# Performance work log

Measured on AMD Instinct MI355X. Metric: run time of the kernel, lower is better.

Reference implementation:

```python
import jax, jax.numpy as jnp
import numpy as np

B, N, C = 4, 4096, 2048
EPS = 1e-5  # torch.nn.LayerNorm default


def setup_inputs() -> dict:
    key = jax.random.key(0)
    kx, = jax.random.split(key, 1)
    x = jax.random.normal(kx, (B, N, C), dtype=jnp.float32)
    gamma = jnp.ones((C,), dtype=jnp.float32)   # LayerNorm weight
    beta = jnp.zeros((C,), dtype=jnp.float32)   # LayerNorm bias
    return {"x": x, "gamma": gamma, "beta": beta}


def reference(x, gamma, beta):
    # The original repeats x to (B,N,N,C), applies a (no-op on the diagonal)
    # triu mask, FFTs every row over C, and extracts the (n,n) diagonal.
    # The diagonal rows are exactly the unmasked originals, so this equals:
    #   LayerNorm(real(fft(x, axis=-1)))
    y = jnp.fft.fft(x, axis=-1).real  # (B,N,C)
    mu = jnp.mean(y, axis=-1, keepdims=True)
    var = jnp.mean(jnp.square(y - mu), axis=-1, keepdims=True)  # biased, as torch LN
    return (y - mu) * jax.lax.rsqrt(var + EPS) * gamma + beta
```

## Files before the change

kernel.cpp:

```cpp
#include <hip/hip_runtime.h>
#include <math.h>


#define TPB 256
#define CD  2048

template<int N_, int S_>
__device__ __forceinline__ void r4_stage(const float2* __restrict__ src,
                                         float2* __restrict__ dst, int t)
{
    const float theta0 = -6.28318530717958647692f / (float)N_;
#pragma unroll
    for (int it = 0; it < 2; ++it) {
        const int b = t + TPB * it;
        const int q = b & (S_ - 1);
        const int p = b / S_;
        float2 x0 = src[b];
        float2 x1 = src[b + 512];
        float2 x2 = src[b + 1024];
        float2 x3 = src[b + 1536];
        float apc_r = x0.x + x2.x, apc_i = x0.y + x2.y;
        float amc_r = x0.x - x2.x, amc_i = x0.y - x2.y;
        float bpd_r = x1.x + x3.x, bpd_i = x1.y + x3.y;
        float bmd_r = x1.x - x3.x, bmd_i = x1.y - x3.y;
        float t0r = apc_r + bpd_r, t0i = apc_i + bpd_i;
        float t2r = apc_r - bpd_r, t2i = apc_i - bpd_i;
        float t1r = amc_r + bmd_i, t1i = amc_i - bmd_r;
        float t3r = amc_r - bmd_i, t3i = amc_i + bmd_r;
        float s1, c1;
        __sincosf(theta0 * (float)p, &s1, &c1);
        const float c2 = c1 * c1 - s1 * s1, s2 = 2.0f * c1 * s1;
        const float c3 = c1 * c2 - s1 * s2, s3 = c1 * s2 + s1 * c2;
        const int o = q + 4 * S_ * p;
        dst[o]          = make_float2(t0r, t0i);
        dst[o + S_]     = make_float2(c1 * t1r - s1 * t1i, c1 * t1i + s1 * t1r);
        dst[o + 2 * S_] = make_float2(c2 * t2r - s2 * t2i, c2 * t2i + s2 * t2r);
        dst[o + 3 * S_] = make_float2(c3 * t3r - s3 * t3i, c3 * t3i + s3 * t3r);
    }
}

__global__ __launch_bounds__(TPB) void fourier_ln_kernel(
    const float* __restrict__ x,
    const float* __restrict__ gamma,
    const float* __restrict__ beta,
    float* __restrict__ out)
{
    __shared__ float2 bufA[CD];
    __shared__ float2 bufB[CD];

    const int t = threadIdx.x;
    const long long row0 = 2LL * (long long)blockIdx.x;
    const long long row1 = row0 + 1;

    const float4* x0 = (const float4*)(x + row0 * CD);
    const float4* x1 = (const float4*)(x + row1 * CD);
#pragma unroll
    for (int i = 0; i < 2; i++) {
        int idx = t + TPB * i;
        float4 a = x0[idx];
        float4 b = x1[idx];
        int base = 4 * idx;
        bufA[base + 0] = make_float2(a.x, b.x);
        bufA[base + 1] = make_float2(a.y, b.y);
        bufA[base + 2] = make_float2(a.z, b.z);
        bufA[base + 3] = make_float2(a.w, b.w);
    }
    __syncthreads();

    r4_stage<2048, 1>(bufA, bufB, t);  __syncthreads();
    r4_stage< 512, 4>(bufB, bufA, t);  __syncthreads();
    r4_stage< 128, 16>(bufA, bufB, t); __syncthreads();
    r4_stage<  32, 64>(bufB, bufA, t); __syncthreads();
    r4_stage<   8, 256>(bufA, bufB, t); __syncthreads();

#pragma unroll
    for (int it = 0; it < 4; ++it) {
        int b = t + TPB * it;
        float2 u = bufB[b];
        float2 v = bufB[b + 1024];
        bufA[b]        = make_float2(u.x + v.x, u.y + v.y);
        bufA[b + 1024] = make_float2(u.x - v.x, u.y - v.y);
    }
    __syncthreads();

    float y0v[8], y1v[8];
    float s0 = 0.f, ss0 = 0.f, s1 = 0.f, ss1 = 0.f;
#pragma unroll
    for (int i = 0; i < 8; i++) {
        int k = t + TPB * i;
        int rv = (CD - k) & (CD - 1);
        float2 zk = bufA[k];
        float2 zr = bufA[rv];
        float a = 0.5f * (zk.x + zr.x);
        float b = 0.5f * (zk.y + zr.y);
        y0v[i] = a; y1v[i] = b;
        s0 += a; ss0 += a * a;
        s1 += b; ss1 += b * b;
    }

#pragma unroll
    for (int off = 32; off > 0; off >>= 1) {
        s0  += __shfl_down(s0,  off, 64);
        ss0 += __shfl_down(ss0, off, 64);
        s1  += __shfl_down(s1,  off, 64);
        ss1 += __shfl_down(ss1, off, 64);
    }
    float* rmem = (float*)bufB;
    const int wave = t >> 6;
    if ((t & 63) == 0) {
        rmem[4 * wave + 0] = s0;
        rmem[4 * wave + 1] = ss0;
        rmem[4 * wave + 2] = s1;
        rmem[4 * wave + 3] = ss1;
    }
    __syncthreads();
    if (t == 0) {
        float S0 = 0.f, SS0 = 0.f, S1 = 0.f, SS1 = 0.f;
#pragma unroll
        for (int w = 0; w < 4; w++) {
            S0  += rmem[4 * w + 0];
            SS0 += rmem[4 * w + 1];
            S1  += rmem[4 * w + 2];
            SS1 += rmem[4 * w + 3];
        }
        const float inv = 1.0f / (float)CD;
        float mu0 = S0 * inv, mu1 = S1 * inv;
        float v0 = SS0 * inv - mu0 * mu0;
        float v1 = SS1 * inv - mu1 * mu1;
        rmem[16] = mu0; rmem[17] = rsqrtf(v0 + 1e-5f);
        rmem[18] = mu1; rmem[19] = rsqrtf(v1 + 1e-5f);
    }
    __syncthreads();
    const float mu0 = rmem[16], r0 = rmem[17];
    const float mu1 = rmem[18], r1 = rmem[19];

    float* o0 = out + row0 * CD;
    float* o1 = out + row1 * CD;
#pragma unroll
    for (int i = 0; i < 8; i++) {
        int k = t + TPB * i;
        float g = gamma[k], be = beta[k];
        o0[k] = (y0v[i] - mu0) * r0 * g + be;
        o1[k] = (y1v[i] - mu1) * r1 * g + be;
    }
}

extern "C" void kernel_launch(void* const* d_in, const int* in_sizes, int n_in,
                              void* d_out, int out_size, void* d_ws, size_t ws_size,
                              hipStream_t stream) {
    (void)in_sizes; (void)n_in; (void)d_ws; (void)ws_size; (void)out_size;
    const float* x     = (const float*)d_in[0];
    const float* gamma = (const float*)d_in[1];
    const float* beta  = (const float*)d_in[2];
    float* out = (float*)d_out;

    const int total_rows = 4 * 4096;
    const int blocks = total_rows / 2;
    fourier_ln_kernel<<<blocks, TPB, 0, stream>>>(x, gamma, beta, out);
}
```

Measured before the change: 231.5 us.

## Replace radix-4 shared-memory FFT with register radix-8 stages and padded LDS

Swaps the five radix-4 stages plus a radix-2 pass, each bouncing through two shared buffers, for three radix-8 register butterflies and a final radix-8 pass (4+2 split). Data moves through one padded shared buffer so LDS accesses avoid bank conflicts. Output and gamma/beta accesses are vectorized to float4, and launch bounds request higher occupancy. The aim is fewer LDS passes and barriers and less shared memory per block, at the cost of more registers per thread and more intricate index math.

```diff
diff --git a/kernel.cpp b/kernel.cpp
--- a/kernel.cpp
+++ b/kernel.cpp
@@ -5,97 +5,135 @@
 #define TPB 256
 #define CD  2048
 
-template<int N_, int S_>
-__device__ __forceinline__ void r4_stage(const float2* __restrict__ src,
-                                         float2* __restrict__ dst, int t)
+__device__ __forceinline__ float2 cadd(float2 a, float2 b){ return make_float2(a.x+b.x, a.y+b.y); }
+__device__ __forceinline__ float2 csub(float2 a, float2 b){ return make_float2(a.x-b.x, a.y-b.y); }
+
+__device__ __forceinline__ void dft8(const float2* z, float2* y)
 {
-    const float theta0 = -6.28318530717958647692f / (float)N_;
-#pragma unroll
-    for (int it = 0; it < 2; ++it) {
-        const int b = t + TPB * it;
-        const int q = b & (S_ - 1);
-        const int p = b / S_;
-        float2 x0 = src[b];
-        float2 x1 = src[b + 512];
-        float2 x2 = src[b + 1024];
-        float2 x3 = src[b + 1536];
-        float apc_r = x0.x + x2.x, apc_i = x0.y + x2.y;
-        float amc_r = x0.x - x2.x, amc_i = x0.y - x2.y;
-        float bpd_r = x1.x + x3.x, bpd_i = x1.y + x3.y;
-        float bmd_r = x1.x - x3.x, bmd_i = x1.y - x3.y;
-        float t0r = apc_r + bpd_r, t0i = apc_i + bpd_i;
-        float t2r = apc_r - bpd_r, t2i = apc_i - bpd_i;
-        float t1r = amc_r + bmd_i, t1i = amc_i - bmd_r;
-        float t3r = amc_r - bmd_i, t3i = amc_i + bmd_r;
-        float s1, c1;
-        __sincosf(theta0 * (float)p, &s1, &c1);
-        const float c2 = c1 * c1 - s1 * s1, s2 = 2.0f * c1 * s1;
-        const float c3 = c1 * c2 - s1 * s2, s3 = c1 * s2 + s1 * c2;
-        const int o = q + 4 * S_ * p;
-        dst[o]          = make_float2(t0r, t0i);
-        dst[o + S_]     = make_float2(c1 * t1r - s1 * t1i, c1 * t1i + s1 * t1r);
-        dst[o + 2 * S_] = make_float2(c2 * t2r - s2 * t2i, c2 * t2i + s2 * t2r);
-        dst[o + 3 * S_] = make_float2(c3 * t3r - s3 * t3i, c3 * t3i + s3 * t3r);
+    const float C8 = 0.70710678118654752440f;
+    float2 a0=cadd(z[0],z[4]), a1=cadd(z[1],z[5]), a2=cadd(z[2],z[6]), a3=cadd(z[3],z[7]);
+    float2 b0=csub(z[0],z[4]), b1=csub(z[1],z[5]), b2=csub(z[2],z[6]), b3=csub(z[3],z[7]);
+    float2 t1=make_float2(C8*(b1.x+b1.y), C8*(b1.y-b1.x));
+    float2 t2=make_float2(b2.y, -b2.x);
+    float2 t3=make_float2(C8*(b3.y-b3.x), -C8*(b3.x+b3.y));
+    {
+        float pr=a0.x+a2.x, pi=a0.y+a2.y, mr=a0.x-a2.x, mi=a0.y-a2.y;
+        float qr=a1.x+a3.x, qi=a1.y+a3.y, nr=a1.x-a3.x, ni=a1.y-a3.y;
+        y[0]=make_float2(pr+qr,pi+qi); y[2]=make_float2(mr+ni,mi-nr);
+        y[4]=make_float2(pr-qr,pi-qi); y[6]=make_float2(mr-ni,mi+nr);
+    }
+    {
+        float pr=b0.x+t2.x, pi=b0.y+t2.y, mr=b0.x-t2.x, mi=b0.y-t2.y;
+        float qr=t1.x+t3.x, qi=t1.y+t3.y, nr=t1.x-t3.x, ni=t1.y-t3.y;
+        y[1]=make_float2(pr+qr,pi+qi); y[3]=make_float2(mr+ni,mi-nr);
+        y[5]=make_float2(pr-qr,pi-qi); y[7]=make_float2(mr-ni,mi+nr);
     }
 }
 
-__global__ __launch_bounds__(TPB) void fourier_ln_kernel(
+template<int S_, int OFFM>
+__device__ __forceinline__ void r8_store(float2* Lw, const float2* y, int p)
+{
+    Lw[0] = y[0];
+    if (S_ == 64 && p == 0) {
+#pragma unroll
+        for (int r = 1; r < 8; ++r) Lw[OFFM*r] = y[r];
+        return;
+    }
+    const float th = -6.28318530717958647692f * ((float)S_ / 2048.0f);
+    float s1, c1;
+    __sincosf(th * (float)p, &s1, &c1);
+    float cr=c1, sr=s1;
+    Lw[OFFM] = make_float2(c1*y[1].x - s1*y[1].y, c1*y[1].y + s1*y[1].x);
+#pragma unroll
+    for (int r = 2; r < 8; ++r) {
+        float cn = cr*c1 - sr*s1, sn = sr*c1 + cr*s1;
+        cr=cn; sr=sn;
+        Lw[OFFM*r] = make_float2(cr*y[r].x - sr*y[r].y, cr*y[r].y + sr*y[r].x);
+    }
+}
+
+__global__ __launch_bounds__(TPB, 8) void fourier_ln_kernel(
     const float* __restrict__ x,
     const float* __restrict__ gamma,
     const float* __restrict__ beta,
     float* __restrict__ out)
 {
-    __shared__ float2 bufA[CD];
-    __shared__ float2 bufB[CD];
+    __shared__ float2 L[2304];
+    __shared__ float rmem[20];
 
-    const int t = threadIdx.x;
+    const int t  = threadIdx.x;
+    const int t8 = t >> 3;
     const long long row0 = 2LL * (long long)blockIdx.x;
-    const long long row1 = row0 + 1;
+    const float* __restrict__ x0 = x + row0 * CD;
+    const float* __restrict__ x1 = x0 + CD;
 
-    const float4* x0 = (const float4*)(x + row0 * CD);
-    const float4* x1 = (const float4*)(x + row1 * CD);
+    float2 z[8], y[8];
 #pragma unroll
-    for (int i = 0; i < 2; i++) {
-        int idx = t + TPB * i;
-        float4 a = x0[idx];
-        float4 b = x1[idx];
-        int base = 4 * idx;
-        bufA[base + 0] = make_float2(a.x, b.x);
-        bufA[base + 1] = make_float2(a.y, b.y);
-        bufA[base + 2] = make_float2(a.z, b.z);
-        bufA[base + 3] = make_float2(a.w, b.w);
+    for (int r = 0; r < 8; ++r) {
+        const int k = t + 256*r;
+        z[r] = make_float2(x0[k], x1[k]);
+    }
+
+    float2* const Lr = L + (t + t8);
+
+    dft8(z, y);
+    r8_store<1, 1>(L + 9*t, y, t);
+    __syncthreads();
+#pragma unroll
+    for (int r = 0; r < 8; ++r) z[r] = Lr[288*r];
+    __syncthreads();
+
+    dft8(z, y);
+    r8_store<8, 9>(L + ((t & 7) + 72*t8), y, t8);
+    __syncthreads();
+#pragma unroll
+    for (int r = 0; r < 8; ++r) z[r] = Lr[288*r];
+    __syncthreads();
+
+    dft8(z, y);
+    {
+        const int q = t & 63, p = t >> 6;
+        r8_store<64, 72>(L + (q + (q >> 3) + 576*p), y, p);
     }
     __syncthreads();
+#pragma unroll
+    for (int r = 0; r < 8; ++r) z[r] = Lr[288*r];
+    __syncthreads();
 
-    r4_stage<2048, 1>(bufA, bufB, t);  __syncthreads();
-    r4_stage< 512, 4>(bufB, bufA, t);  __syncthreads();
-    r4_stage< 128, 16>(bufA, bufB, t); __syncthreads();
-    r4_stage<  32, 64>(bufB, bufA, t); __syncthreads();
-    r4_stage<   8, 256>(bufA, bufB, t); __syncthreads();
-
+    float2 Z[8];
+    {
+        float pr=z[0].x+z[4].x, pi=z[0].y+z[4].y, mr=z[0].x-z[4].x, mi=z[0].y-z[4].y;
+        float qr=z[2].x+z[6].x, qi=z[2].y+z[6].y, nr=z[2].x-z[6].x, ni=z[2].y-z[6].y;
+        Z[0]=make_float2(pr+qr,pi+qi); Z[2]=make_float2(mr+ni,mi-nr);
+        Z[4]=make_float2(pr-qr,pi-qi); Z[6]=make_float2(mr-ni,mi+nr);
+    }
+    {
+        float pr=z[1].x+z[5].x, pi=z[1].y+z[5].y, mr=z[1].x-z[5].x, mi=z[1].y-z[5].y;
+        float qr=z[3].x+z[7].x, qi=z[3].y+z[7].y, nr=z[3].x-z[7].x, ni=z[3].y-z[7].y;
+        Z[1]=make_float2(pr+qr,pi+qi); Z[3]=make_float2(mr+ni,mi-nr);
+        Z[5]=make_float2(pr-qr,pi-qi); Z[7]=make_float2(mr-ni,mi+nr);
+    }
 #pragma unroll
-    for (int it = 0; it < 4; ++it) {
-        int b = t + TPB * it;
-        float2 u = bufB[b];
-        float2 v = bufB[b + 1024];
-        bufA[b]        = make_float2(u.x + v.x, u.y + v.y);
-        bufA[b + 1024] = make_float2(u.x - v.x, u.y - v.y);
-    }
+    for (int j = 0; j < 8; ++j) Lr[288*j] = Z[j];
     __syncthreads();
 
     float y0v[8], y1v[8];
-    float s0 = 0.f, ss0 = 0.f, s1 = 0.f, ss1 = 0.f;
+    float s0=0.f, ss0=0.f, s1=0.f, ss1=0.f;
+    const float2* const Ls = L + (4*t + (t >> 1));
 #pragma unroll
-    for (int i = 0; i < 8; i++) {
-        int k = t + TPB * i;
-        int rv = (CD - k) & (CD - 1);
-        float2 zk = bufA[k];
-        float2 zr = bufA[rv];
-        float a = 0.5f * (zk.x + zr.x);
-        float b = 0.5f * (zk.y + zr.y);
-        y0v[i] = a; y1v[i] = b;
-        s0 += a; ss0 += a * a;
-        s1 += b; ss1 += b * b;
+    for (int h = 0; h < 2; ++h) {
+#pragma unroll
+        for (int c = 0; c < 4; ++c) {
+            const int k  = 4*t + 1024*h + c;
+            const int rv = (CD - k) & (CD - 1);
+            float2 zk = Ls[c + 1152*h];
+            float2 zr = L[rv + (rv >> 3)];
+            float a = 0.5f*(zk.x + zr.x);
+            float b = 0.5f*(zk.y + zr.y);
+            const int i = 4*h + c;
+            y0v[i]=a; y1v[i]=b;
+            s0+=a; ss0+=a*a; s1+=b; ss1+=b*b;
+        }
     }
 
 #pragma unroll
@@ -105,43 +143,40 @@
         s1  += __shfl_down(s1,  off, 64);
         ss1 += __shfl_down(ss1, off, 64);
     }
-    float* rmem = (float*)bufB;
     const int wave = t >> 6;
     if ((t & 63) == 0) {
-        rmem[4 * wave + 0] = s0;
-        rmem[4 * wave + 1] = ss0;
-        rmem[4 * wave + 2] = s1;
-        rmem[4 * wave + 3] = ss1;
+        rmem[4*wave+0]=s0; rmem[4*wave+1]=ss0; rmem[4*wave+2]=s1; rmem[4*wave+3]=ss1;
     }
     __syncthreads();
     if (t == 0) {
-        float S0 = 0.f, SS0 = 0.f, S1 = 0.f, SS1 = 0.f;
+        float S0=0.f, SS0=0.f, S1=0.f, SS1=0.f;
 #pragma unroll
-        for (int w = 0; w < 4; w++) {
-            S0  += rmem[4 * w + 0];
-            SS0 += rmem[4 * w + 1];
-            S1  += rmem[4 * w + 2];
-            SS1 += rmem[4 * w + 3];
+        for (int w = 0; w < 4; ++w) {
+            S0+=rmem[4*w+0]; SS0+=rmem[4*w+1]; S1+=rmem[4*w+2]; SS1+=rmem[4*w+3];
         }
-        const float inv = 1.0f / (float)CD;
-        float mu0 = S0 * inv, mu1 = S1 * inv;
-        float v0 = SS0 * inv - mu0 * mu0;
-        float v1 = SS1 * inv - mu1 * mu1;
-        rmem[16] = mu0; rmem[17] = rsqrtf(v0 + 1e-5f);
-        rmem[18] = mu1; rmem[19] = rsqrtf(v1 + 1e-5f);
+        const float inv = 1.0f/(float)CD;
+        float m0=S0*inv, m1=S1*inv;
+        rmem[16]=m0; rmem[17]=rsqrtf(SS0*inv - m0*m0 + 1e-5f);
+        rmem[18]=m1; rmem[19]=rsqrtf(SS1*inv - m1*m1 + 1e-5f);
     }
     __syncthreads();
-    const float mu0 = rmem[16], r0 = rmem[17];
-    const float mu1 = rmem[18], r1 = rmem[19];
+    const float mu0=rmem[16], r0=rmem[17], mu1=rmem[18], r1=rmem[19];
 
-    float* o0 = out + row0 * CD;
-    float* o1 = out + row1 * CD;
+    const float4* gv = (const float4*)gamma;
+    const float4* bv = (const float4*)beta;
+    float4* o0 = (float4*)(out + row0*CD);
+    float4* o1 = (float4*)(out + (row0+1)*CD);
 #pragma unroll
-    for (int i = 0; i < 8; i++) {
-        int k = t + TPB * i;
-        float g = gamma[k], be = beta[k];
-        o0[k] = (y0v[i] - mu0) * r0 * g + be;
-        o1[k] = (y1v[i] - mu1) * r1 * g + be;
+    for (int h = 0; h < 2; ++h) {
+        const int i4 = t + 256*h;
+        float4 g  = gv[i4];
+        float4 be = bv[i4];
+        float4 v0, v1;
+        v0.x=(y0v[4*h+0]-mu0)*r0*g.x+be.x; v0.y=(y0v[4*h+1]-mu0)*r0*g.y+be.y;
+        v0.z=(y0v[4*h+2]-mu0)*r0*g.z+be.z; v0.w=(y0v[4*h+3]-mu0)*r0*g.w+be.w;
+        v1.x=(y1v[4*h+0]-mu1)*r1*g.x+be.x; v1.y=(y1v[4*h+1]-mu1)*r1*g.y+be.y;
+        v1.z=(y1v[4*h+2]-mu1)*r1*g.z+be.z; v1.w=(y1v[4*h+3]-mu1)*r1*g.w+be.w;
+        o0[i4]=v0; o1[i4]=v1;
     }
 }
 
```

Measured after the change: 232.7 us. Within noise of the previous version (+0.5%).
